# Kernel optimization log

Hardware: AMD Instinct MI355X
Metric: run time of the kernel (lower is better)

## Reference

```python
import jax, jax.numpy as jnp
import numpy as np


def _sigma(x):
    # sigma(x) = x if x>=0 else exp(x)-1  (ELU, alpha=1)
    return jnp.where(x >= 0, x, jnp.expm1(x))


def setup_inputs() -> dict:
    key = jax.random.key(0)
    ks = jax.random.split(key, 7)
    B, L, D = 4, 4096, 1024
    s = 0.02
    return {
        "query": jax.random.normal(ks[0], (B, L, D), jnp.float32),
        "key_in": jax.random.normal(ks[1], (B, L, D), jnp.float32),
        "value": jax.random.normal(ks[2], (B, L, D), jnp.float32),
        "Wq": jax.random.normal(ks[3], (D, D), jnp.float32) * s,
        "bq": jnp.zeros((D,), jnp.float32),
        "Wk": jax.random.normal(ks[4], (D, D), jnp.float32) * s,
        "bk": jnp.zeros((D,), jnp.float32),
        "Wv": jax.random.normal(ks[5], (D, D), jnp.float32) * s,
        "bv": jnp.zeros((D,), jnp.float32),
        "Wo": jax.random.normal(ks[6], (D, D), jnp.float32) * s,
        "bo": jnp.zeros((D,), jnp.float32),
        "beta": jnp.array(1.0, jnp.float32),
        "seq_count": 8,
        "num_heads": 16,
        "use_mask": 1,
        "delta_rule": 1,
    }


def reference(query, key_in, value, Wq, bq, Wk, bk, Wv, bv, Wo, bo, beta,
              seq_count, num_heads, use_mask, delta_rule):
    B, L, D = query.shape
    H = num_heads
    dh = D // H
    S = L // seq_count
    scale = 1.0 / jnp.sqrt(jnp.float32(dh))

    def split_heads(x):
        # [B,L,D] -> [B,H,C,S,dh]
        return x.reshape(B, seq_count, S, H, dh).transpose(0, 3, 1, 2, 4)

    q = split_heads(query @ Wq + bq)
    k = split_heads(key_in @ Wk + bk)
    v = split_heads(value @ Wv + bv)

    g = jax.nn.sigmoid(beta)
    causal = (1.0 - jnp.tril(jnp.ones((S, S), jnp.float32))) * 1e-9 if use_mask else 0.0

    # z init broadcast to [B,H,dh,dh]: identical math to source since first-step
    # numerators (Memory=0) are zero regardless of denominator.
    M0 = jnp.zeros((B, H, dh, dh), q.dtype)
    z0 = jnp.zeros((B, H, dh, dh), q.dtype)

    def step(carry, seg):
        M, z = carry
        qi, ki, vi = seg  # each [B,H,S,dh]
        sqi = _sigma(qi)
        ski = _sigma(ki)
        # memory readout with PRE-update Memory
        A = (sqi @ M) / (sqi @ z + 1e-6)
        val = vi
        if delta_rule:
            val = vi - (ski @ M) / (ski @ z + 1e-6)
        M = M + jnp.einsum('bhsd,bhse->bhde', ski, val)
        z = z + jnp.sum(ski, axis=-2, keepdims=True)
        # local softmax attention within segment
        logits = jnp.einsum('bhsd,bhtd->bhst', qi, ki) * scale + causal
        dot = jnp.einsum('bhst,bhtd->bhsd', jax.nn.softmax(logits, axis=-1), vi)
        return (M, z), g * A + (1.0 - g) * dot

    segs = (q.transpose(2, 0, 1, 3, 4),
            k.transpose(2, 0, 1, 3, 4),
            v.transpose(2, 0, 1, 3, 4))  # [C,B,H,S,dh]
    _, outs = jax.lax.scan(step, (M0, z0), segs)  # outs: [C,B,H,S,dh]
    # tf.concat(axis=1) over segments -> [B, C*H, S, dh], then reshape/transpose
    O = outs.transpose(1, 0, 2, 3, 4).reshape(B, D, L)
    O = O.transpose(0, 2, 1)  # [B, L, D]
    return O @ Wo + bo
```

## Files before the change

### kernel.cpp

```cpp
#include <hip/hip_runtime.h>
#include <math.h>

#define Bz 4
#define Lz 4096
#define Dz 1024
#define Hz 16
#define Cz 8
#define Sz 512
#define DHz 64

typedef __bf16 bf16x8 __attribute__((ext_vector_type(8)));
typedef float f32x16 __attribute__((ext_vector_type(16)));

__device__ __forceinline__ float sigmaf(float x) {
    return x >= 0.f ? x : expm1f(x);
}

__device__ __forceinline__ unsigned pkbf(float a, float b) {
    unsigned r;
    asm("v_cvt_pk_bf16_f32 %0, %1, %2" : "=v"(r) : "v"(a), "v"(b));
    return r;
}

__global__ __launch_bounds__(256) void wt_kernel(
    const float* __restrict__ W, unsigned short* __restrict__ dst)
{
    __shared__ float Ls[64][65];
    const int tid = threadIdx.x;
    const int n0 = blockIdx.x * 64, k0 = blockIdx.y * 64;
#pragma unroll
    for (int i = 0; i < 4; ++i) {
        int idx = i * 256 + tid;
        int r = idx >> 4, c4 = (idx & 15) * 4;
        float4 t = *(const float4*)&W[(size_t)(k0 + r) * 1024 + n0 + c4];
        Ls[r][c4] = t.x; Ls[r][c4 + 1] = t.y; Ls[r][c4 + 2] = t.z; Ls[r][c4 + 3] = t.w;
    }
    __syncthreads();
    const int n = tid >> 2, j0 = (tid & 3) * 16;
    unsigned uh[8], ul[8];
#pragma unroll
    for (int j = 0; j < 8; ++j) {
        float a = Ls[j0 + 2 * j][n], b = Ls[j0 + 2 * j + 1][n];
        unsigned h = pkbf(a, b);
        float ra = a - __uint_as_float(h << 16);
        float rb = b - __uint_as_float(h & 0xffff0000u);
        uh[j] = h; ul[j] = pkbf(ra, rb);
    }
    unsigned short* op = dst + (size_t)(n0 + n) * 1024 + k0 + j0;
    uint4 o;
    o.x = uh[0]; o.y = uh[1]; o.z = uh[2]; o.w = uh[3]; *(uint4*)op = o;
    o.x = uh[4]; o.y = uh[5]; o.z = uh[6]; o.w = uh[7]; *(uint4*)(op + 8) = o;
    op += 1048576;
    o.x = ul[0]; o.y = ul[1]; o.z = ul[2]; o.w = ul[3]; *(uint4*)op = o;
    o.x = ul[4]; o.y = ul[5]; o.z = ul[6]; o.w = ul[7]; *(uint4*)(op + 8) = o;
}

__global__ __launch_bounds__(256) void xtt_kernel(
    const float* __restrict__ XT, unsigned short* __restrict__ dst)
{
    __shared__ float Ls[64][65];
    const int tid = threadIdx.x;
    const int b = blockIdx.z, e0 = blockIdx.y * 64, l0 = blockIdx.x * 64;
#pragma unroll
    for (int i = 0; i < 4; ++i) {
        int idx = i * 256 + tid;
        int r = idx >> 4, c4 = (idx & 15) * 4;
        float4 t = *(const float4*)&XT[((size_t)b * 1024 + e0 + r) * 4096 + l0 + c4];
        Ls[r][c4] = t.x; Ls[r][c4 + 1] = t.y; Ls[r][c4 + 2] = t.z; Ls[r][c4 + 3] = t.w;
    }
    __syncthreads();
    const int l = tid >> 2, j0 = (tid & 3) * 16;
    unsigned uh[8], ul[8];
#pragma unroll
    for (int j = 0; j < 8; ++j) {
        float a = Ls[j0 + 2 * j][l], b2 = Ls[j0 + 2 * j + 1][l];
        unsigned h = pkbf(a, b2);
        float ra = a - __uint_as_float(h << 16);
        float rb = b2 - __uint_as_float(h & 0xffff0000u);
        uh[j] = h; ul[j] = pkbf(ra, rb);
    }
    unsigned short* op = dst + ((size_t)(b * 4096 + l0 + l)) * 1024 + e0 + j0;
    uint4 o;
    o.x = uh[0]; o.y = uh[1]; o.z = uh[2]; o.w = uh[3]; *(uint4*)op = o;
    o.x = uh[4]; o.y = uh[5]; o.z = uh[6]; o.w = uh[7]; *(uint4*)(op + 8) = o;
    op += 16777216;
    o.x = ul[0]; o.y = ul[1]; o.z = ul[2]; o.w = ul[3]; *(uint4*)op = o;
    o.x = ul[4]; o.y = ul[5]; o.z = ul[6]; o.w = ul[7]; *(uint4*)(op + 8) = o;
}

template<bool ASPLIT, bool FULL4>
__global__ __launch_bounds__(256) void mm_split(
    const float* __restrict__ Af32, const unsigned short* __restrict__ Abf,
    const unsigned short* __restrict__ Bt,
    const float* __restrict__ bias, float* __restrict__ C)
{
    __shared__ __align__(16) unsigned short Ah[128 * 64];
    __shared__ __align__(16) unsigned short Al[128 * 64];
    __shared__ __align__(16) unsigned short Bh[128 * 64];
    __shared__ __align__(16) unsigned short Bl[128 * 64];
    const int tid = threadIdx.x;
    const int m0 = blockIdx.y * 128, n0 = blockIdx.x * 128;
    const int lane = tid & 63, w = tid >> 6;
    const int lq = lane & 31, hi = lane >> 5;
    const int wm = (w >> 1) * 64, wn = (w & 1) * 64;

    f32x16 acc[2][2];
#pragma unroll
    for (int i = 0; i < 2; ++i)
#pragma unroll
        for (int j = 0; j < 2; ++j)
#pragma unroll
            for (int r = 0; r < 16; ++r) acc[i][j][r] = 0.f;

    for (int kb = 0; kb < 1024; kb += 64) {
        __syncthreads();
        if constexpr (ASPLIT) {
#pragma unroll
            for (int i = 0; i < 8; ++i) {
                int idx = i * 256 + tid;
                int r = idx >> 4, fq = idx & 15;
                float4 a = *(const float4*)(Af32 + (size_t)(m0 + r) * 1024 + kb + fq * 4);
                unsigned h0 = pkbf(a.x, a.y), h1 = pkbf(a.z, a.w);
                float rx = a.x - __uint_as_float(h0 << 16);
                float ry = a.y - __uint_as_float(h0 & 0xffff0000u);
                float rz = a.z - __uint_as_float(h1 << 16);
                float rw = a.w - __uint_as_float(h1 & 0xffff0000u);
                unsigned l0 = pkbf(rx, ry), l1 = pkbf(rz, rw);
                int boff = r * 128 + ((fq * 8) ^ ((r & 7) << 4));
                uint2 th; th.x = h0; th.y = h1;
                uint2 tl; tl.x = l0; tl.y = l1;
                *(uint2*)((char*)Ah + boff) = th;
                *(uint2*)((char*)Al + boff) = tl;
            }
        } else {
#pragma unroll
            for (int p = 0; p < 2; ++p) {
                const unsigned short* ap = Abf + (size_t)p * 16777216 + (size_t)m0 * 1024 + kb;
                unsigned short* dst = p ? Al : Ah;
#pragma unroll
                for (int i = 0; i < 4; ++i) {
                    int idx = i * 256 + tid;
                    int r = idx >> 3, uq = idx & 7;
                    uint4 d = *(const uint4*)(ap + (size_t)r * 1024 + uq * 8);
                    *(uint4*)((char*)dst + r * 128 + ((uq * 16) ^ ((r & 7) << 4))) = d;
                }
            }
        }
#pragma unroll
        for (int p = 0; p < 2; ++p) {
            const unsigned short* bp = Bt + (size_t)p * 1048576 + (size_t)n0 * 1024 + kb;
            unsigned short* dst = p ? Bl : Bh;
#pragma unroll
            for (int i = 0; i < 4; ++i) {
                int idx = i * 256 + tid;
                int r = idx >> 3, uq = idx & 7;
                uint4 d = *(const uint4*)(bp + (size_t)r * 1024 + uq * 8);
                *(uint4*)((char*)dst + r * 128 + ((uq * 16) ^ ((r & 7) << 4))) = d;
            }
        }
        __syncthreads();
#pragma unroll
        for (int kt = 0; kt < 4; ++kt) {
            bf16x8 fah[2], fal[2], fbh[2], fbl[2];
            const int cb = kt * 32 + hi * 16;
#pragma unroll
            for (int mb = 0; mb < 2; ++mb) {
                int r = wm + mb * 32 + lq;
                int off = r * 128 + (cb ^ ((r & 7) << 4));
                fah[mb] = *(const bf16x8*)((const char*)Ah + off);
                fal[mb] = *(const bf16x8*)((const char*)Al + off);
            }
#pragma unroll
            for (int nb = 0; nb < 2; ++nb) {
                int r = wn + nb * 32 + lq;
                int off = r * 128 + (cb ^ ((r & 7) << 4));
                fbh[nb] = *(const bf16x8*)((const char*)Bh + off);
                fbl[nb] = *(const bf16x8*)((const char*)Bl + off);
            }
#pragma unroll
            for (int mb = 0; mb < 2; ++mb)
#pragma unroll
                for (int nb = 0; nb < 2; ++nb) {
                    acc[mb][nb] = __builtin_amdgcn_mfma_f32_32x32x16_bf16(fah[mb], fbh[nb], acc[mb][nb], 0, 0, 0);
                    acc[mb][nb] = __builtin_amdgcn_mfma_f32_32x32x16_bf16(fah[mb], fbl[nb], acc[mb][nb], 0, 0, 0);
                    acc[mb][nb] = __builtin_amdgcn_mfma_f32_32x32x16_bf16(fal[mb], fbh[nb], acc[mb][nb], 0, 0, 0);
                    if constexpr (FULL4)
                        acc[mb][nb] = __builtin_amdgcn_mfma_f32_32x32x16_bf16(fal[mb], fbl[nb], acc[mb][nb], 0, 0, 0);
                }
        }
    }
#pragma unroll
    for (int mb = 0; mb < 2; ++mb)
#pragma unroll
        for (int nb = 0; nb < 2; ++nb) {
            int n = n0 + wn + nb * 32 + lq;
            float bn = bias[n];
#pragma unroll
            for (int r = 0; r < 16; ++r) {
                int m = m0 + wm + mb * 32 + (r & 3) + 8 * (r >> 2) + 4 * hi;
                C[(size_t)m * 1024 + n] = acc[mb][nb][r] + bn;
            }
        }
}

__global__ __launch_bounds__(256) void vt_kernel(
    const float* __restrict__ v, unsigned short* __restrict__ vth)
{
    const int b = blockIdx.z, h = blockIdx.y, l0 = blockIdx.x * 64;
    const int tid = threadIdx.x;
    __shared__ float Ls[64][65];
#pragma unroll
    for (int it = 0; it < 4; ++it) {
        int idx = it * 256 + tid;
        int r = idx >> 4, c4 = (idx & 15) * 4;
        float4 t = *(const float4*)&v[((size_t)b * Lz + l0 + r) * Dz + h * DHz + c4];
        Ls[r][c4] = t.x; Ls[r][c4 + 1] = t.y; Ls[r][c4 + 2] = t.z; Ls[r][c4 + 3] = t.w;
    }
    __syncthreads();
    const int d = tid >> 2, j0 = (tid & 3) * 16;
    unsigned u[8];
#pragma unroll
    for (int j = 0; j < 8; ++j)
        u[j] = pkbf(Ls[j0 + 2 * j][d], Ls[j0 + 2 * j + 1][d]);
    unsigned short* op = vth + ((size_t)(b * Hz + h) * 64 + d) * Lz + l0 + j0;
    uint4 o0; o0.x = u[0]; o0.y = u[1]; o0.z = u[2]; o0.w = u[3];
    uint4 o1; o1.x = u[4]; o1.y = u[5]; o1.z = u[6]; o1.w = u[7];
    *(uint4*)op = o0;
    *(uint4*)(op + 8) = o1;
}

__global__ __launch_bounds__(256) void attn_kernel(
    const float* __restrict__ q, const float* __restrict__ k,
    const unsigned short* __restrict__ vth,
    const float* __restrict__ beta, float* __restrict__ XT)
{
    const int bh = blockIdx.z; const int b = bh >> 4, h = bh & 15;
    const int c = blockIdx.y;
    const int qt = blockIdx.x;
    const int tid = threadIdx.x;
    const int lane = tid & 63;
    const int w = tid >> 6;
    const int lq = lane & 31;
    const int hi = lane >> 5;
    const float g = 1.f / (1.f + __expf(-beta[0]));

    __shared__ __align__(16) unsigned short Qs[128 * 64];
    __shared__ __align__(16) unsigned short Ks[64 * 64];
    __shared__ __align__(16) unsigned short Vs[64 * 64];
    __shared__ float lsum_lds[128];

    const size_t rowb = (size_t)b * Lz * Dz + (size_t)h * DHz;

    {
        const int r = tid >> 2, c4 = tid & 3;
#pragma unroll
        for (int p = 0; p < 2; ++p) {
            int rr = p * 64 + r;
            const float* qp = q + rowb + (size_t)(c * Sz + qt * 128 + rr) * Dz + c4 * 16;
            float4 f0 = ((const float4*)qp)[0];
            float4 f1 = ((const float4*)qp)[1];
            float4 f2 = ((const float4*)qp)[2];
            float4 f3 = ((const float4*)qp)[3];
            uint4 u0, u1;
            u0.x = pkbf(f0.x, f0.y); u0.y = pkbf(f0.z, f0.w);
            u0.z = pkbf(f1.x, f1.y); u0.w = pkbf(f1.z, f1.w);
            u1.x = pkbf(f2.x, f2.y); u1.y = pkbf(f2.z, f2.w);
            u1.z = pkbf(f3.x, f3.y); u1.w = pkbf(f3.z, f3.w);
            int base = rr * 128;
            *(uint4*)((char*)Qs + base + ((c4 * 32)      ^ ((rr & 7) << 4))) = u0;
            *(uint4*)((char*)Qs + base + ((c4 * 32 + 16) ^ ((rr & 7) << 4))) = u1;
        }
    }
    __syncthreads();
    bf16x8 qf[4];
#pragma unroll
    for (int ck = 0; ck < 4; ++ck) {
        int rr = w * 32 + lq;
        qf[ck] = *(const bf16x8*)((const char*)Qs + rr * 128 + ((ck * 32 + hi * 16) ^ ((rr & 7) << 4)));
    }

    f32x16 acc0, acc1;
#pragma unroll
    for (int r = 0; r < 16; ++r) { acc0[r] = 0.f; acc1[r] = 0.f; }
    float lsum = 0.f;

    for (int kt = 0; kt < 8; ++kt) {
        __syncthreads();
        {
            const int r = tid >> 2, c4 = tid & 3;
            const float* kp = k + rowb + (size_t)(c * Sz + kt * 64 + r) * Dz + c4 * 16;
            float4 f0 = ((const float4*)kp)[0];
            float4 f1 = ((const float4*)kp)[1];
            float4 f2 = ((const float4*)kp)[2];
            float4 f3 = ((const float4*)kp)[3];
            uint4 u0, u1;
            u0.x = pkbf(f0.x, f0.y); u0.y = pkbf(f0.z, f0.w);
            u0.z = pkbf(f1.x, f1.y); u0.w = pkbf(f1.z, f1.w);
            u1.x = pkbf(f2.x, f2.y); u1.y = pkbf(f2.z, f2.w);
            u1.z = pkbf(f3.x, f3.y); u1.w = pkbf(f3.z, f3.w);
            int base = r * 128;
            *(uint4*)((char*)Ks + base + ((c4 * 32)      ^ ((r & 7) << 4))) = u0;
            *(uint4*)((char*)Ks + base + ((c4 * 32 + 16) ^ ((r & 7) << 4))) = u1;
            const unsigned short* vp = vth + ((size_t)(b * Hz + h) * 64 + r) * Lz + c * Sz + kt * 64 + c4 * 16;
            uint4 v0 = ((const uint4*)vp)[0];
            uint4 v1 = ((const uint4*)vp)[1];
            *(uint4*)((char*)Vs + base + ((c4 * 32)      ^ ((r & 7) << 4))) = v0;
            *(uint4*)((char*)Vs + base + ((c4 * 32 + 16) ^ ((r & 7) << 4))) = v1;
        }
        __syncthreads();

        bf16x8 pA[4];
#pragma unroll
        for (int tb = 0; tb < 2; ++tb) {
            f32x16 pt;
#pragma unroll
            for (int r = 0; r < 16; ++r) pt[r] = 0.f;
#pragma unroll
            for (int ck = 0; ck < 4; ++ck) {
                int rr = tb * 32 + lq;
                bf16x8 ka = *(const bf16x8*)((const char*)Ks + rr * 128 + ((ck * 32 + hi * 16) ^ ((rr & 7) << 4)));
                pt = __builtin_amdgcn_mfma_f32_32x32x16_bf16(ka, qf[ck], pt, 0, 0, 0);
            }
            float p[16];
#pragma unroll
            for (int r = 0; r < 16; ++r) { p[r] = __expf(pt[r] * 0.125f); lsum += p[r]; }
#pragma unroll
            for (int cc = 0; cc < 2; ++cc) {
                unsigned u0 = pkbf(p[8 * cc + 0], p[8 * cc + 1]);
                unsigned u1 = pkbf(p[8 * cc + 2], p[8 * cc + 3]);
                unsigned u2 = pkbf(p[8 * cc + 4], p[8 * cc + 5]);
                unsigned u3 = pkbf(p[8 * cc + 6], p[8 * cc + 7]);
                asm volatile("v_permlane32_swap_b32 %0, %1" : "+v"(u0), "+v"(u2));
                asm volatile("v_permlane32_swap_b32 %0, %1" : "+v"(u1), "+v"(u3));
                union { unsigned u[4]; bf16x8 v; } pa;
                pa.u[0] = u0; pa.u[1] = u1; pa.u[2] = u2; pa.u[3] = u3;
                pA[tb * 2 + cc] = pa.v;
            }
        }
#pragma unroll
        for (int ck = 0; ck < 4; ++ck) {
            int r0 = lq;
            bf16x8 vf0 = *(const bf16x8*)((const char*)Vs + r0 * 128 + ((ck * 32 + hi * 16) ^ ((r0 & 7) << 4)));
            acc0 = __builtin_amdgcn_mfma_f32_32x32x16_bf16(pA[ck], vf0, acc0, 0, 0, 0);
            int r1 = 32 + lq;
            bf16x8 vf1 = *(const bf16x8*)((const char*)Vs + r1 * 128 + ((ck * 32 + hi * 16) ^ ((r1 & 7) << 4)));
            acc1 = __builtin_amdgcn_mfma_f32_32x32x16_bf16(pA[ck], vf1, acc1, 0, 0, 0);
        }
    }

    lsum += __shfl_xor(lsum, 32);
    if (hi == 0) lsum_lds[w * 32 + lq] = lsum;
    __syncthreads();

    const float invg = 1.f - g;
#pragma unroll
    for (int r = 0; r < 16; ++r) {
        int ql = (r & 3) + 8 * (r >> 2) + 4 * hi;
        float sc = invg / lsum_lds[w * 32 + ql];
        int s = qt * 128 + w * 32 + ql;
        int e = c * 128 + h * 8 + (s >> 6);
        float* xp = XT + ((size_t)b * Dz + e) * Lz + (s & 63) * 64;
        xp[lq]      = acc0[r] * sc;
        xp[32 + lq] = acc1[r] * sc;
    }
}

__global__ __launch_bounds__(256) void scan_s1(
    const float* __restrict__ k, const float* __restrict__ v,
    float* __restrict__ Mpre, float* __restrict__ zpre)
{
    const int bx = blockIdx.x;
    const int bh = bx >> 3, es = bx & 7;
    const int b = bh >> 4, h = bh & 15;
    const int tid = threadIdx.x;
    const int el = tid & 7;
    const int rs = tid >> 3;
    const int eg = es * 8 + el;

    __shared__ float ks[64][68];
    __shared__ float vs2[64][8];

    float Mreg[64];
#pragma unroll
    for (int d = 0; d < 64; ++d) Mreg[d] = 0.f;
    float zreg = 0.f;

    const size_t boff = (size_t)b * Lz * Dz + h * DHz;

    for (int c = 0; c < Cz; ++c) {
        {
            float* mp = Mpre + ((size_t)(bh * Cz + c) * 64) * 64;
#pragma unroll
            for (int j = 0; j < 2; ++j) {
                int d = rs * 2 + j;
                mp[(size_t)d * 64 + eg] = Mreg[d];
            }
            if (rs == 0) zpre[(size_t)(bh * Cz + c) * 64 + eg] = zreg;
        }
        float mdelta[2] = {0.f, 0.f};
        float zd = 0.f;

        for (int ch = 0; ch < 8; ++ch) {
            const int s0 = c * Sz + ch * 64;
            __syncthreads();
#pragma unroll
            for (int it = 0; it < 4; ++it) {
                int idx = it * 256 + tid;
                int r = idx >> 4, f = (idx & 15) * 4;
                float4 t = *(const float4*)(k + boff + (size_t)(s0 + r) * Dz + f);
                ks[r][f + 0] = sigmaf(t.x); ks[r][f + 1] = sigmaf(t.y);
                ks[r][f + 2] = sigmaf(t.z); ks[r][f + 3] = sigmaf(t.w);
            }
            {
                int r = tid >> 2, f = (tid & 3) * 2;
                float2 t = *(const float2*)(v + boff + (size_t)(s0 + r) * Dz + es * 8 + f);
                *(float2*)&vs2[r][f] = t;
            }
            __syncthreads();
#pragma unroll
            for (int j = 0; j < 2; ++j) {
                const int sl = rs * 2 + j;
                float numk = 0.f, ssk = 0.f;
#pragma unroll
                for (int d = 0; d < 64; d += 4) {
                    float4 kk = *(const float4*)&ks[sl][d];
                    numk += kk.x * Mreg[d] + kk.y * Mreg[d + 1]
                          + kk.z * Mreg[d + 2] + kk.w * Mreg[d + 3];
                    ssk += kk.x + kk.y + kk.z + kk.w;
                }
                vs2[sl][el] = vs2[sl][el] - numk / (ssk * zreg + 1e-6f);
            }
            __syncthreads();
            for (int sl = 0; sl < 64; ++sl) {
                float vv = vs2[sl][el];
                float2 kk = *(const float2*)&ks[sl][rs * 2];
                mdelta[0] += kk.x * vv; mdelta[1] += kk.y * vv;
                zd += ks[sl][eg];
            }
        }
        __syncthreads();
#pragma unroll
        for (int j = 0; j < 2; ++j) vs2[rs * 2 + j][el] = mdelta[j];
        __syncthreads();
#pragma unroll
        for (int d = 0; d < 64; ++d) Mreg[d] += vs2[d][el];
        zreg += zd;
    }
}

__global__ __launch_bounds__(256) void scan_s2(
    const float* __restrict__ q, const float* __restrict__ Mpre,
    const float* __restrict__ zpre, const float* __restrict__ beta,
    float* __restrict__ XT)
{
    const int bh = blockIdx.z; const int b = bh >> 4, h = bh & 15;
    const int c = blockIdx.y;
    const int tile = blockIdx.x;
    const int tid = threadIdx.x;
    const int lane = tid & 63;
    const int w = tid >> 6;
    const float g = 1.f / (1.f + __expf(-beta[0]));

    __shared__ float qs[64][68];

    float Mreg[64];
    const float* mp = Mpre + ((size_t)(bh * Cz + c) * 64) * 64;
#pragma unroll
    for (int d = 0; d < 64; ++d) Mreg[d] = mp[(size_t)d * 64 + lane];
    const float zv = zpre[(size_t)(bh * Cz + c) * 64 + lane];

    const size_t boff = (size_t)b * Lz * Dz + h * DHz;
    const int s0 = c * Sz + tile * 64;
#pragma unroll
    for (int it = 0; it < 4; ++it) {
        int idx = it * 256 + tid;
        int r = idx >> 4, f = (idx & 15) * 4;
        float4 t = *(const float4*)(q + boff + (size_t)(s0 + r) * Dz + f);
        qs[r][f + 0] = sigmaf(t.x); qs[r][f + 1] = sigmaf(t.y);
        qs[r][f + 2] = sigmaf(t.z); qs[r][f + 3] = sigmaf(t.w);
    }
    __syncthreads();

    const int e_out = c * 128 + h * 8 + tile;
    float* xp = XT + ((size_t)b * Dz + e_out) * Lz;
    for (int i = 0; i < 16; ++i) {
        const int sl = w * 16 + i;
        float num = 0.f, ssq = 0.f;
#pragma unroll
        for (int d = 0; d < 64; d += 4) {
            float4 qq = *(const float4*)&qs[sl][d];
            num += qq.x * Mreg[d] + qq.y * Mreg[d + 1]
                 + qq.z * Mreg[d + 2] + qq.w * Mreg[d + 3];
            ssq += qq.x + qq.y + qq.z + qq.w;
        }
        float A = num / (ssq * zv + 1e-6f);
        size_t xoff = (size_t)sl * 64 + lane;
        xp[xoff] += g * A;
    }
}

extern "C" void kernel_launch(void* const* d_in, const int* in_sizes, int n_in,
                              void* d_out, int out_size, void* d_ws, size_t ws_size,
                              hipStream_t stream)
{
    (void)in_sizes; (void)n_in; (void)out_size; (void)ws_size;
    const float* query  = (const float*)d_in[0];
    const float* key_in = (const float*)d_in[1];
    const float* value  = (const float*)d_in[2];
    const float* Wq = (const float*)d_in[3];
    const float* bq = (const float*)d_in[4];
    const float* Wk = (const float*)d_in[5];
    const float* bk = (const float*)d_in[6];
    const float* Wv = (const float*)d_in[7];
    const float* bv = (const float*)d_in[8];
    const float* Wo = (const float*)d_in[9];
    const float* bo = (const float*)d_in[10];
    const float* beta = (const float*)d_in[11];
    float* out = (float*)d_out;

    const size_t NE = (size_t)Bz * Lz * Dz;
    const size_t NM = (size_t)64 * Cz * 64 * 64;
    float* qb = (float*)d_ws;
    float* kb = qb + NE;
    float* vb = kb + NE;
    float* Mpre = vb + NE;
    float* zpre = Mpre + NM;
    float* XT = vb;

    unsigned short* u0  = (unsigned short*)d_out;
    unsigned short* Wtq = u0;
    unsigned short* Wtk = u0 + 2 * 1048576;
    unsigned short* Wtv = u0 + 4 * 1048576;
    unsigned short* vth = u0 + 6 * 1048576;
    unsigned short* Wto = (unsigned short*)kb;
    unsigned short* XTt = (unsigned short*)qb;

    wt_kernel<<<dim3(16, 16), 256, 0, stream>>>(Wq, Wtq);
    wt_kernel<<<dim3(16, 16), 256, 0, stream>>>(Wk, Wtk);
    wt_kernel<<<dim3(16, 16), 256, 0, stream>>>(Wv, Wtv);
    mm_split<true, true><<<dim3(8, 128), 256, 0, stream>>>(query,  nullptr, Wtq, bq, qb);
    mm_split<true, true><<<dim3(8, 128), 256, 0, stream>>>(key_in, nullptr, Wtk, bk, kb);
    mm_split<true, true><<<dim3(8, 128), 256, 0, stream>>>(value,  nullptr, Wtv, bv, vb);
    vt_kernel<<<dim3(Lz / 64, Hz, Bz), 256, 0, stream>>>(vb, vth);
    scan_s1<<<dim3(512), 256, 0, stream>>>(kb, vb, Mpre, zpre);
    attn_kernel<<<dim3(4, Cz, Bz * Hz), 256, 0, stream>>>(qb, kb, vth, beta, XT);
    scan_s2<<<dim3(8, Cz, Bz * Hz), 256, 0, stream>>>(qb, Mpre, zpre, beta, XT);
    wt_kernel<<<dim3(16, 16), 256, 0, stream>>>(Wo, Wto);
    xtt_kernel<<<dim3(Lz / 64, Dz / 64, Bz), 256, 0, stream>>>(XT, XTt);
    mm_split<false, false><<<dim3(8, 128), 256, 0, stream>>>(nullptr, XTt, Wto, bo, out);
}
```

Before: 1.882 ms.

## Prefetch next chunk in scan_s1, transpose v in LDS, optionally precompute ELU(k)

The sequential scan kernel now loads the next 64-row chunk of k and v into registers while the current chunk is being processed. The v tile is kept transposed in shared memory so the outer-product accumulation can read float4 vectors. When the workspace is large enough, a separate elementwise kernel applies the ELU to k ahead of time so the scan skips that work. The trade-off is higher register pressure and an extra full-tensor read/write pass for the precomputed ELU.

```diff
diff --git a/kernel.cpp b/kernel.cpp
--- a/kernel.cpp
+++ b/kernel.cpp
@@ -227,6 +227,19 @@
     uint4 o1; o1.x = u[4]; o1.y = u[5]; o1.z = u[6]; o1.w = u[7];
     *(uint4*)op = o0;
     *(uint4*)(op + 8) = o1;
+}
+
+__global__ __launch_bounds__(256) void sigk_kernel(
+    const float* __restrict__ k, float* __restrict__ sk)
+{
+    const size_t n4 = (size_t)Bz * Lz * Dz / 4;
+    size_t i = (size_t)blockIdx.x * 256 + threadIdx.x;
+    const size_t stride = (size_t)gridDim.x * 256;
+    for (; i < n4; i += stride) {
+        float4 t = ((const float4*)k)[i];
+        t.x = sigmaf(t.x); t.y = sigmaf(t.y); t.z = sigmaf(t.z); t.w = sigmaf(t.w);
+        ((float4*)sk)[i] = t;
+    }
 }
 
 __global__ __launch_bounds__(256) void attn_kernel(
@@ -365,8 +378,18 @@
     }
 }
 
+#define S1_LOAD(S0_) do {                                                            \
+    _Pragma("unroll")                                                                \
+    for (int it_ = 0; it_ < 4; ++it_) {                                              \
+        int r_ = it_ * 16 + (tid >> 4);                                              \
+        ka[it_] = *(const float4*)(ksrc + boff + (size_t)((S0_) + r_) * Dz + (tid & 15) * 4); \
+    }                                                                                \
+    va = *(const float2*)(v + boff + (size_t)((S0_) + (tid >> 2)) * Dz + es * 8 + (tid & 3) * 2); \
+} while (0)
+
+template<bool PRE>
 __global__ __launch_bounds__(256) void scan_s1(
-    const float* __restrict__ k, const float* __restrict__ v,
+    const float* __restrict__ ksrc, const float* __restrict__ v,
     float* __restrict__ Mpre, float* __restrict__ zpre)
 {
     const int bx = blockIdx.x;
@@ -378,7 +401,7 @@
     const int eg = es * 8 + el;
 
     __shared__ float ks[64][68];
-    __shared__ float vs2[64][8];
+    __shared__ float vsT[8][68];
 
     float Mreg[64];
 #pragma unroll
@@ -397,24 +420,27 @@
             }
             if (rs == 0) zpre[(size_t)(bh * Cz + c) * 64 + eg] = zreg;
         }
-        float mdelta[2] = {0.f, 0.f};
+        float mdelta0 = 0.f, mdelta1 = 0.f;
         float zd = 0.f;
 
+        float4 ka[4]; float2 va;
+        S1_LOAD(c * Sz);
+
         for (int ch = 0; ch < 8; ++ch) {
-            const int s0 = c * Sz + ch * 64;
             __syncthreads();
 #pragma unroll
             for (int it = 0; it < 4; ++it) {
-                int idx = it * 256 + tid;
-                int r = idx >> 4, f = (idx & 15) * 4;
-                float4 t = *(const float4*)(k + boff + (size_t)(s0 + r) * Dz + f);
-                ks[r][f + 0] = sigmaf(t.x); ks[r][f + 1] = sigmaf(t.y);
-                ks[r][f + 2] = sigmaf(t.z); ks[r][f + 3] = sigmaf(t.w);
+                int r = it * 16 + (tid >> 4), f = (tid & 15) * 4;
+                float4 t = ka[it];
+                if constexpr (!PRE) {
+                    t.x = sigmaf(t.x); t.y = sigmaf(t.y);
+                    t.z = sigmaf(t.z); t.w = sigmaf(t.w);
+                }
+                *(float4*)&ks[r][f] = t;
             }
             {
                 int r = tid >> 2, f = (tid & 3) * 2;
-                float2 t = *(const float2*)(v + boff + (size_t)(s0 + r) * Dz + es * 8 + f);
-                *(float2*)&vs2[r][f] = t;
+                vsT[f][r] = va.x; vsT[f + 1][r] = va.y;
             }
             __syncthreads();
 #pragma unroll
@@ -428,22 +454,49 @@
                           + kk.z * Mreg[d + 2] + kk.w * Mreg[d + 3];
                     ssk += kk.x + kk.y + kk.z + kk.w;
                 }
-                vs2[sl][el] = vs2[sl][el] - numk / (ssk * zreg + 1e-6f);
-            }
+                vsT[el][sl] = vsT[el][sl] - numk / (ssk * zreg + 1e-6f);
+            }
+            if (ch < 7) S1_LOAD(c * Sz + (ch + 1) * 64);
             __syncthreads();
-            for (int sl = 0; sl < 64; ++sl) {
-                float vv = vs2[sl][el];
-                float2 kk = *(const float2*)&ks[sl][rs * 2];
-                mdelta[0] += kk.x * vv; mdelta[1] += kk.y * vv;
-                zd += ks[sl][eg];
+#pragma unroll
+            for (int sl4 = 0; sl4 < 16; ++sl4) {
+                float4 vv4 = *(const float4*)&vsT[el][sl4 * 4];
+                {
+                    const int sl = sl4 * 4;
+                    float2 kk = *(const float2*)&ks[sl][rs * 2];
+                    mdelta0 += kk.x * vv4.x; mdelta1 += kk.y * vv4.x;
+                    zd += ks[sl][eg];
+                }
+                {
+                    const int sl = sl4 * 4 + 1;
+                    float2 kk = *(const float2*)&ks[sl][rs * 2];
+                    mdelta0 += kk.x * vv4.y; mdelta1 += kk.y * vv4.y;
+                    zd += ks[sl][eg];
+                }
+                {
+                    const int sl = sl4 * 4 + 2;
+                    float2 kk = *(const float2*)&ks[sl][rs * 2];
+                    mdelta0 += kk.x * vv4.z; mdelta1 += kk.y * vv4.z;
+                    zd += ks[sl][eg];
+                }
+                {
+                    const int sl = sl4 * 4 + 3;
+                    float2 kk = *(const float2*)&ks[sl][rs * 2];
+                    mdelta0 += kk.x * vv4.w; mdelta1 += kk.y * vv4.w;
+                    zd += ks[sl][eg];
+                }
             }
         }
         __syncthreads();
-#pragma unroll
-        for (int j = 0; j < 2; ++j) vs2[rs * 2 + j][el] = mdelta[j];
+        vsT[el][rs * 2]     = mdelta0;
+        vsT[el][rs * 2 + 1] = mdelta1;
         __syncthreads();
 #pragma unroll
-        for (int d = 0; d < 64; ++d) Mreg[d] += vs2[d][el];
+        for (int d = 0; d < 64; d += 4) {
+            float4 md = *(const float4*)&vsT[el][d];
+            Mreg[d] += md.x; Mreg[d + 1] += md.y;
+            Mreg[d + 2] += md.z; Mreg[d + 3] += md.w;
+        }
         zreg += zd;
     }
 }
@@ -503,7 +556,7 @@
                               void* d_out, int out_size, void* d_ws, size_t ws_size,
                               hipStream_t stream)
 {
-    (void)in_sizes; (void)n_in; (void)out_size; (void)ws_size;
+    (void)in_sizes; (void)n_in; (void)out_size;
     const float* query  = (const float*)d_in[0];
     const float* key_in = (const float*)d_in[1];
     const float* value  = (const float*)d_in[2];
@@ -520,12 +573,15 @@
 
     const size_t NE = (size_t)Bz * Lz * Dz;
     const size_t NM = (size_t)64 * Cz * 64 * 64;
+    const size_t NZ = (size_t)64 * Cz * 64;
     float* qb = (float*)d_ws;
     float* kb = qb + NE;
     float* vb = kb + NE;
     float* Mpre = vb + NE;
     float* zpre = Mpre + NM;
     float* XT = vb;
+    float* sk = zpre + NZ;
+    const bool big = ws_size >= (4 * NE + NM + NZ) * sizeof(float);
 
     unsigned short* u0  = (unsigned short*)d_out;
     unsigned short* Wtq = u0;
@@ -542,7 +598,12 @@
     mm_split<true, true><<<dim3(8, 128), 256, 0, stream>>>(key_in, nullptr, Wtk, bk, kb);
     mm_split<true, true><<<dim3(8, 128), 256, 0, stream>>>(value,  nullptr, Wtv, bv, vb);
     vt_kernel<<<dim3(Lz / 64, Hz, Bz), 256, 0, stream>>>(vb, vth);
-    scan_s1<<<dim3(512), 256, 0, stream>>>(kb, vb, Mpre, zpre);
+    if (big) {
+        sigk_kernel<<<dim3(2048), 256, 0, stream>>>(kb, sk);
+        scan_s1<true><<<dim3(512), 256, 0, stream>>>(sk, vb, Mpre, zpre);
+    } else {
+        scan_s1<false><<<dim3(512), 256, 0, stream>>>(kb, vb, Mpre, zpre);
+    }
     attn_kernel<<<dim3(4, Cz, Bz * Hz), 256, 0, stream>>>(qb, kb, vth, beta, XT);
     scan_s2<<<dim3(8, Cz, Bz * Hz), 256, 0, stream>>>(qb, Mpre, zpre, beta, XT);
     wt_kernel<<<dim3(16, 16), 256, 0, stream>>>(Wo, Wto);
```

Result: faster. 1.671 ms (-11.2%).
